# Kernel optimization log

Hardware: AMD Instinct MI355X
Metric: run time of the kernel (lower is better)

## Reference

```python
import jax, jax.numpy as jnp
import numpy as np

N_NODES = 100000
N_EDGES = 1600000
IN_DIM, HID_DIM, OUT_DIM = 256, 128, 64


def gcn_conv(x, row, col, deg_inv_sqrt, W, b, n_nodes):
    # PyG GCNConv: transform first, then degree-normalized aggregation.
    h = x @ W  # [N, d_out]
    norm = deg_inv_sqrt[row] * deg_inv_sqrt[col]  # [E]
    msg = h[row] * norm[:, None]  # gather + scale, [E, d_out]
    out = jax.ops.segment_sum(msg, col, num_segments=n_nodes)  # scatter-add
    return out + b


def setup_inputs() -> dict:
    key = jax.random.key(0)
    k1, k2, k3, k4 = jax.random.split(key, 4)
    x = jax.random.normal(k1, (N_NODES, IN_DIM), dtype=jnp.float32)
    edge_index = jax.random.randint(k2, (2, N_EDGES), 0, N_NODES, dtype=jnp.int64)
    # Glorot-ish init for weights, zeros for bias (PyG GCNConv default)
    W1 = jax.random.normal(k3, (IN_DIM, HID_DIM), dtype=jnp.float32) * (1.0 / np.sqrt(IN_DIM))
    b1 = jnp.zeros((HID_DIM,), dtype=jnp.float32)
    W2 = jax.random.normal(k4, (HID_DIM, OUT_DIM), dtype=jnp.float32) * (1.0 / np.sqrt(HID_DIM))
    b2 = jnp.zeros((OUT_DIM,), dtype=jnp.float32)
    return {"x": x, "edge_index": edge_index, "W1": W1, "b1": b1, "W2": W2, "b2": b2}


def reference(x, edge_index, W1, b1, W2, b2):
    n = x.shape[0]
    # add self-loops (PyG GCNConv default add_self_loops=True)
    loops = jnp.arange(n, dtype=edge_index.dtype)
    row = jnp.concatenate([edge_index[0], loops])  # source
    col = jnp.concatenate([edge_index[1], loops])  # target
    # symmetric normalization: deg computed at target nodes incl. self-loops
    deg = jax.ops.segment_sum(jnp.ones_like(col, dtype=x.dtype), col, num_segments=n)
    deg_inv_sqrt = jnp.where(deg > 0, jax.lax.rsqrt(jnp.maximum(deg, 1e-12)), 0.0)

    h = jax.nn.relu(gcn_conv(x, row, col, deg_inv_sqrt, W1, b1, n))
    # dropout is identity in eval mode
    out = gcn_conv(h, row, col, deg_inv_sqrt, W2, b2, n)
    return out
```

## Files before the change

kernel.cpp:

```cpp
#include <hip/hip_runtime.h>
#include <hip/hip_fp16.h>


constexpr int IN_DIM  = 256;
constexpr int HID_DIM = 128;
constexpr int OUT_DIM = 64;
constexpr int CAP     = 64;
constexpr int BCHUNK  = 16384;

typedef short bf16x8 __attribute__((ext_vector_type(8)));
typedef float f32x16 __attribute__((ext_vector_type(16)));

__device__ __forceinline__ void split2(float v, short& hi, short& lo) {
    unsigned b = __builtin_bit_cast(unsigned, v);
    unsigned r = (b + 0x7FFFu + ((b >> 16) & 1u)) >> 16;
    hi = (short)r;
    float hf = __builtin_bit_cast(float, r << 16);
    float res = v - hf;
    lo = (short)(__builtin_bit_cast(unsigned, res) >> 16);
}


template <int K, int N>
__device__ __forceinline__ void wprep_one(const float* __restrict__ W,
                                          short* __restrict__ hi,
                                          short* __restrict__ lo, int tid) {
    constexpr int F = N / 32;
    const int l    = tid & 63;
    const int f    = (tid >> 6) % F;
    const int sIdx = tid / (64 * F);
    const int c    = f * 32 + (l & 31);
    const size_t off = ((size_t)(sIdx * F + f) * 64 + l) * 8;
#pragma unroll
    for (int j = 0; j < 8; ++j) {
        int k = sIdx * 16 + 8 * (l >> 5) + j;
        short h, lw;
        split2(W[(size_t)k * N + c], h, lw);
        hi[off + j] = h;
        lo[off + j] = lw;
    }
}

__global__ void k_prep(const float* __restrict__ W1, const float* __restrict__ W2,
                       int* __restrict__ cursor,
                       short* __restrict__ w1hi, short* __restrict__ w1lo,
                       short* __restrict__ w2hi, short* __restrict__ w2lo, int n) {
    int tid = blockIdx.x * 256 + threadIdx.x;
    if (tid < n) cursor[tid] = 0;
    if (tid < (IN_DIM / 16) * (HID_DIM / 32) * 64)
        wprep_one<IN_DIM, HID_DIM>(W1, w1hi, w1lo, tid);
    if (tid < (HID_DIM / 16) * (OUT_DIM / 32) * 64)
        wprep_one<HID_DIM, OUT_DIM>(W2, w2hi, w2lo, tid);
}


__global__ __launch_bounds__(256)
void k_bucket(const int* __restrict__ row, const int* __restrict__ col,
              int* __restrict__ cursor, int* __restrict__ srow,
              int E, int nPerSlice) {
    const int slice = blockIdx.x & 7;
    const int chunk = blockIdx.x >> 3;
    const int lo    = slice * nPerSlice;
    const int hi    = lo + nPerSlice;
    const int base  = chunk * BCHUNK;
#pragma unroll
    for (int it = 0; it < BCHUNK / 1024; ++it) {
        const int idx = base + it * 1024 + threadIdx.x * 4;
        if (idx < E) {
            const int4 c4 = *reinterpret_cast<const int4*>(&col[idx]);
            const bool m0 = c4.x >= lo && c4.x < hi;
            const bool m1 = c4.y >= lo && c4.y < hi;
            const bool m2 = c4.z >= lo && c4.z < hi;
            const bool m3 = c4.w >= lo && c4.w < hi;
            if (m0 | m1 | m2 | m3) {
                const int4 r4 = *reinterpret_cast<const int4*>(&row[idx]);
                if (m0) { int p = atomicAdd(&cursor[c4.x], 1); if (p < CAP) srow[(size_t)c4.x * CAP + p] = r4.x; }
                if (m1) { int p = atomicAdd(&cursor[c4.y], 1); if (p < CAP) srow[(size_t)c4.y * CAP + p] = r4.y; }
                if (m2) { int p = atomicAdd(&cursor[c4.z], 1); if (p < CAP) srow[(size_t)c4.z * CAP + p] = r4.z; }
                if (m3) { int p = atomicAdd(&cursor[c4.w], 1); if (p < CAP) srow[(size_t)c4.w * CAP + p] = r4.w; }
            }
        }
    }
}


template <int K, int N>
__global__ __launch_bounds__(256)
void k_gemm_mfma(const float* __restrict__ A, const short* __restrict__ Bhi,
                 const short* __restrict__ Blo, __half* __restrict__ C, int M) {
    constexpr int F = N / 32;
    constexpr int S = K / 32;
    __shared__ short Ah[128 * 40];
    __shared__ short Al[128 * 40];

    const int t      = threadIdx.x;
    const int lane   = t & 63;
    const int w      = t >> 6;
    const int blockM = blockIdx.x * 128;

    f32x16 acc[F];
#pragma unroll
    for (int f = 0; f < F; ++f)
#pragma unroll
        for (int e = 0; e < 16; ++e) acc[f][e] = 0.0f;

    float4 rv[4];
    auto LOAD = [&](int s) {
#pragma unroll
        for (int p = 0; p < 4; ++p) {
            int idx = t + 256 * p;
            int m   = idx >> 3;
            int kc  = (idx & 7) * 4;
            int gr  = blockM + m;
            rv[p] = (gr < M)
                ? *reinterpret_cast<const float4*>(&A[(size_t)gr * K + s * 32 + kc])
                : make_float4(0.f, 0.f, 0.f, 0.f);
        }
    };
    auto STORE_LDS = [&]() {
#pragma unroll
        for (int p = 0; p < 4; ++p) {
            int idx = t + 256 * p;
            int m   = idx >> 3;
            int kc  = (idx & 7) * 4;
            short h0, h1, h2, h3, l0, l1, l2, l3;
            split2(rv[p].x, h0, l0);
            split2(rv[p].y, h1, l1);
            split2(rv[p].z, h2, l2);
            split2(rv[p].w, h3, l3);
            *reinterpret_cast<short4*>(&Ah[m * 40 + kc]) = make_short4(h0, h1, h2, h3);
            *reinterpret_cast<short4*>(&Al[m * 40 + kc]) = make_short4(l0, l1, l2, l3);
        }
    };

    LOAD(0);
    STORE_LDS();
    __syncthreads();

    for (int s = 0; s < S; ++s) {
        if (s + 1 < S) LOAD(s + 1);
#pragma unroll
        for (int ss = 0; ss < 2; ++ss) {
            const int sIdx  = s * 2 + ss;
            const int aoff  = (w * 32 + (lane & 31)) * 40 + ss * 16 + (lane >> 5) * 8;
            const bf16x8 ah = *reinterpret_cast<const bf16x8*>(&Ah[aoff]);
            const bf16x8 al = *reinterpret_cast<const bf16x8*>(&Al[aoff]);
#pragma unroll
            for (int f = 0; f < F; ++f) {
                const size_t off = ((size_t)(sIdx * F + f) * 64 + lane) * 8;
                const bf16x8 bh = *reinterpret_cast<const bf16x8*>(Bhi + off);
                const bf16x8 bl = *reinterpret_cast<const bf16x8*>(Blo + off);
                acc[f] = __builtin_amdgcn_mfma_f32_32x32x16_bf16(ah, bh, acc[f], 0, 0, 0);
                acc[f] = __builtin_amdgcn_mfma_f32_32x32x16_bf16(ah, bl, acc[f], 0, 0, 0);
                acc[f] = __builtin_amdgcn_mfma_f32_32x32x16_bf16(al, bh, acc[f], 0, 0, 0);
            }
        }
        __syncthreads();
        if (s + 1 < S) {
            STORE_LDS();
            __syncthreads();
        }
    }

#pragma unroll
    for (int f = 0; f < F; ++f) {
        const int c = f * 32 + (lane & 31);
#pragma unroll
        for (int r = 0; r < 16; ++r) {
            int rowl = (r & 3) + 8 * (r >> 2) + 4 * (lane >> 5);
            int gm   = blockM + w * 32 + rowl;
            if (gm < M) C[(size_t)gm * N + c] = __float2half(acc[f][r]);
        }
    }
}


template <int D, bool RELU>
__global__ __launch_bounds__(256)
void k_agg(const int* __restrict__ cnt, const int* __restrict__ srow,
           const __half* __restrict__ h, const float* __restrict__ bias,
           float* __restrict__ out, int n) {
    const int lane = threadIdx.x & 63;
    const int wave = threadIdx.x >> 6;
    const int i    = blockIdx.x * 4 + wave;
    if (i >= n) return;

    int degv = cnt[i];
    const int deg = __builtin_amdgcn_readfirstlane(degv > CAP ? CAP : degv);
    const float di   = rsqrtf((float)(deg + 1));
    const float self = di * di;

    int   r_l = 0;
    float w_l = 0.f;
    if (lane < deg) {
        r_l = srow[(size_t)i * CAP + lane];
        w_l = rsqrtf((float)(cnt[r_l] + 1)) * di;
    }

    if constexpr (D == 128) {
        const float2  bb = *reinterpret_cast<const float2*>(&bias[lane * 2]);
        const __half2 hs = *reinterpret_cast<const __half2*>(&h[(size_t)i * D + lane * 2]);
        const float2  fs = __half22float2(hs);
        float ax = bb.x + fs.x * self;
        float ay = bb.y + fs.y * self;
        int j = 0;
        for (; j + 8 <= deg; j += 8) {
            int rr[8]; float ww[8]; __half2 hv[8];
#pragma unroll
            for (int u = 0; u < 8; ++u) { rr[u] = __shfl(r_l, j + u); ww[u] = __shfl(w_l, j + u); }
#pragma unroll
            for (int u = 0; u < 8; ++u)
                hv[u] = *reinterpret_cast<const __half2*>(&h[(size_t)rr[u] * D + lane * 2]);
#pragma unroll
            for (int u = 0; u < 8; ++u) {
                float2 f2 = __half22float2(hv[u]);
                ax += f2.x * ww[u];
                ay += f2.y * ww[u];
            }
        }
        for (; j < deg; ++j) {
            const int   r = __shfl(r_l, j);
            const float w = __shfl(w_l, j);
            float2 f2 = __half22float2(
                *reinterpret_cast<const __half2*>(&h[(size_t)r * D + lane * 2]));
            ax += f2.x * w;
            ay += f2.y * w;
        }
        if (RELU) { ax = fmaxf(ax, 0.f); ay = fmaxf(ay, 0.f); }
        *reinterpret_cast<float2*>(&out[(size_t)i * D + lane * 2]) = make_float2(ax, ay);
    } else {
        float a = bias[lane] + __half2float(h[(size_t)i * D + lane]) * self;
        int j = 0;
        for (; j + 8 <= deg; j += 8) {
            int rr[8]; float ww[8]; __half hv[8];
#pragma unroll
            for (int u = 0; u < 8; ++u) { rr[u] = __shfl(r_l, j + u); ww[u] = __shfl(w_l, j + u); }
#pragma unroll
            for (int u = 0; u < 8; ++u) hv[u] = h[(size_t)rr[u] * D + lane];
#pragma unroll
            for (int u = 0; u < 8; ++u) a += __half2float(hv[u]) * ww[u];
        }
        for (; j < deg; ++j) {
            const int   r = __shfl(r_l, j);
            const float w = __shfl(w_l, j);
            a += __half2float(h[(size_t)r * D + lane]) * w;
        }
        if (RELU) a = fmaxf(a, 0.f);
        out[(size_t)i * D + lane] = a;
    }
}


extern "C" void kernel_launch(void* const* d_in, const int* in_sizes, int n_in,
                              void* d_out, int out_size, void* d_ws, size_t ws_size,
                              hipStream_t stream) {
    const float* x  = (const float*)d_in[0];
    const int*   ei = (const int*)d_in[1];
    const float* W1 = (const float*)d_in[2];
    const float* b1 = (const float*)d_in[3];
    const float* W2 = (const float*)d_in[4];
    const float* b2 = (const float*)d_in[5];

    const int N = in_sizes[0] / IN_DIM;
    const int E = in_sizes[1] / 2;
    const int* row = ei;
    const int* col = ei + E;

    int*    cursor = (int*)d_ws;
    int*    srow   = cursor + N;
    __half* h1     = (__half*)(srow + (size_t)N * CAP);
    float*  agg1   = (float*)(h1 + (size_t)N * HID_DIM);
    __half* h2     = (__half*)(agg1 + (size_t)N * HID_DIM);
    short*  w1hi   = (short*)(h2 + (size_t)N * OUT_DIM);
    short*  w1lo   = w1hi + IN_DIM * HID_DIM;
    short*  w2hi   = w1lo + IN_DIM * HID_DIM;
    short*  w2lo   = w2hi + HID_DIM * OUT_DIM;
    float*  out    = (float*)d_out;

    const int nPerSlice = (N + 7) / 8;
    const int nChunks   = (E + BCHUNK - 1) / BCHUNK;

    k_prep<<<(N + 255) / 256, 256, 0, stream>>>(W1, W2, cursor,
                                                w1hi, w1lo, w2hi, w2lo, N);

    k_bucket<<<nChunks * 8, 256, 0, stream>>>(row, col, cursor, srow, E, nPerSlice);

    k_gemm_mfma<IN_DIM, HID_DIM>
        <<<(N + 127) / 128, 256, 0, stream>>>(x, w1hi, w1lo, h1, N);
    k_agg<HID_DIM, true><<<(N + 3) / 4, 256, 0, stream>>>(
        cursor, srow, h1, b1, agg1, N);

    k_gemm_mfma<HID_DIM, OUT_DIM>
        <<<(N + 127) / 128, 256, 0, stream>>>(agg1, w2hi, w2lo, h2, N);
    k_agg<OUT_DIM, false><<<(N + 3) / 4, 256, 0, stream>>>(
        cursor, srow, h2, b2, out, N);
}
```

Measured before the change: 454.5 us.

## Fuse edge bucketing and first GEMM into one interleaved kernel launch

Merges the independent edge-bucketing pass and the first layer GEMM into a single kernel. Block indices are interleaved in groups of 64 bucket blocks plus 8 GEMM blocks, so the atomic-heavy bucketing and the MFMA GEMM run concurrently on the GPU. The bucket chunk size shrinks so that enough bucket blocks exist to pair with the GEMM blocks. Every block now reserves the GEMM's shared memory, which may lower occupancy for the bucket blocks, and smaller chunks mean more blocks each rescanning the column array per slice.

```diff
diff --git a/kernel.cpp b/kernel.cpp
--- a/kernel.cpp
+++ b/kernel.cpp
@@ -6,7 +6,8 @@
 constexpr int HID_DIM = 128;
 constexpr int OUT_DIM = 64;
 constexpr int CAP     = 64;
-constexpr int BCHUNK  = 16384;
+constexpr int BCHUNK  = 2048;
+constexpr int GROUP   = 72;
 
 typedef short bf16x8 __attribute__((ext_vector_type(8)));
 typedef float f32x16 __attribute__((ext_vector_type(16)));
@@ -54,15 +55,15 @@
 }
 
 
-__global__ __launch_bounds__(256)
-void k_bucket(const int* __restrict__ row, const int* __restrict__ col,
-              int* __restrict__ cursor, int* __restrict__ srow,
-              int E, int nPerSlice) {
-    const int slice = blockIdx.x & 7;
-    const int chunk = blockIdx.x >> 3;
-    const int lo    = slice * nPerSlice;
-    const int hi    = lo + nPerSlice;
-    const int base  = chunk * BCHUNK;
+__device__ __forceinline__ void bucket_body(const int* __restrict__ row,
+                                            const int* __restrict__ col,
+                                            int* __restrict__ cursor,
+                                            int* __restrict__ srow,
+                                            int E, int nPerSlice,
+                                            int slice, int chunk) {
+    const int lo   = slice * nPerSlice;
+    const int hi   = lo + nPerSlice;
+    const int base = chunk * BCHUNK;
 #pragma unroll
     for (int it = 0; it < BCHUNK / 1024; ++it) {
         const int idx = base + it * 1024 + threadIdx.x * 4;
@@ -85,18 +86,17 @@
 
 
 template <int K, int N>
-__global__ __launch_bounds__(256)
-void k_gemm_mfma(const float* __restrict__ A, const short* __restrict__ Bhi,
-                 const short* __restrict__ Blo, __half* __restrict__ C, int M) {
+__device__ __forceinline__ void gemm_body(const float* __restrict__ A,
+                                          const short* __restrict__ Bhi,
+                                          const short* __restrict__ Blo,
+                                          __half* __restrict__ C, int M,
+                                          int blockM, short* Ah, short* Al) {
     constexpr int F = N / 32;
     constexpr int S = K / 32;
-    __shared__ short Ah[128 * 40];
-    __shared__ short Al[128 * 40];
-
-    const int t      = threadIdx.x;
-    const int lane   = t & 63;
-    const int w      = t >> 6;
-    const int blockM = blockIdx.x * 128;
+
+    const int t    = threadIdx.x;
+    const int lane = t & 63;
+    const int w    = t >> 6;
 
     f32x16 acc[F];
 #pragma unroll
@@ -175,6 +175,38 @@
 }
 
 
+__global__ __launch_bounds__(256)
+void k_fused(const int* __restrict__ row, const int* __restrict__ col,
+             int* __restrict__ cursor, int* __restrict__ srow,
+             int E, int nPerSlice, int bucketBlocks,
+             const float* __restrict__ A, const short* __restrict__ Bhi,
+             const short* __restrict__ Blo, __half* __restrict__ C,
+             int M, int gemmBlocks) {
+    __shared__ short Ah[128 * 40];
+    __shared__ short Al[128 * 40];
+    const int g = blockIdx.x / GROUP;
+    const int j = blockIdx.x % GROUP;
+    if (j < 64) {
+        const int bIdx = g * 64 + j;
+        if (bIdx < bucketBlocks)
+            bucket_body(row, col, cursor, srow, E, nPerSlice, j & 7, bIdx >> 3);
+    } else {
+        const int mblk = g * 8 + (j - 64);
+        if (mblk < gemmBlocks)
+            gemm_body<IN_DIM, HID_DIM>(A, Bhi, Blo, C, M, mblk * 128, Ah, Al);
+    }
+}
+
+template <int K, int N>
+__global__ __launch_bounds__(256)
+void k_gemm_mfma(const float* __restrict__ A, const short* __restrict__ Bhi,
+                 const short* __restrict__ Blo, __half* __restrict__ C, int M) {
+    __shared__ short Ah[128 * 40];
+    __shared__ short Al[128 * 40];
+    gemm_body<K, N>(A, Bhi, Blo, C, M, blockIdx.x * 128, Ah, Al);
+}
+
+
 template <int D, bool RELU>
 __global__ __launch_bounds__(256)
 void k_agg(const int* __restrict__ cnt, const int* __restrict__ srow,
@@ -277,16 +309,20 @@
     short*  w2lo   = w2hi + HID_DIM * OUT_DIM;
     float*  out    = (float*)d_out;
 
-    const int nPerSlice = (N + 7) / 8;
-    const int nChunks   = (E + BCHUNK - 1) / BCHUNK;
+    const int nPerSlice    = (N + 7) / 8;
+    const int nChunks      = (E + BCHUNK - 1) / BCHUNK;
+    const int bucketBlocks = nChunks * 8;
+    const int gemmBlocks   = (N + 127) / 128;
+    const int nGroups      = max((bucketBlocks + 63) / 64,
+                                 (gemmBlocks + 7) / 8);
 
     k_prep<<<(N + 255) / 256, 256, 0, stream>>>(W1, W2, cursor,
                                                 w1hi, w1lo, w2hi, w2lo, N);
 
-    k_bucket<<<nChunks * 8, 256, 0, stream>>>(row, col, cursor, srow, E, nPerSlice);
-
-    k_gemm_mfma<IN_DIM, HID_DIM>
-        <<<(N + 127) / 128, 256, 0, stream>>>(x, w1hi, w1lo, h1, N);
+    k_fused<<<nGroups * GROUP, 256, 0, stream>>>(
+        row, col, cursor, srow, E, nPerSlice, bucketBlocks,
+        x, w1hi, w1lo, h1, N, gemmBlocks);
+
     k_agg<HID_DIM, true><<<(N + 3) / 4, 256, 0, stream>>>(
         cursor, srow, h1, b1, agg1, N);
 
```

Result: slower. 486.2 us (+7.0%).
